# Kernel optimization log

Hardware: AMD Instinct MI355X
Metric: run time of the kernel (lower is better)

Reference implementation:

```python
import jax, jax.numpy as jnp
import numpy as np

L, B, S, H, NH, FF = 4, 16, 512, 768, 12, 3072
D = H // NH
SCALE = D ** -0.5
EPS = 1e-5


def _ln(x, g, b):
    m = jnp.mean(x, axis=-1, keepdims=True)
    v = jnp.mean((x - m) ** 2, axis=-1, keepdims=True)
    return (x - m) * jax.lax.rsqrt(v + EPS) * g + b


def setup_inputs() -> dict:
    key = jax.random.key(0)
    ks = jax.random.split(key, 16)
    def n(k, shape, s=0.02):
        return jax.random.normal(k, shape, dtype=jnp.float32) * s
    return {
        "x": jax.random.normal(ks[0], (B, S, H), dtype=jnp.float32),
        "attn_bias": jax.random.normal(ks[1], (B, NH, S, S), dtype=jnp.float32) * 0.1,
        "ln1_g": jnp.ones((L, H), jnp.float32), "ln1_b": jnp.zeros((L, H), jnp.float32),
        "wq": n(ks[2], (L, H, H)), "bq": jnp.zeros((L, H), jnp.float32),
        "wk": n(ks[3], (L, H, H)), "bk": jnp.zeros((L, H), jnp.float32),
        "wv": n(ks[4], (L, H, H)), "bv": jnp.zeros((L, H), jnp.float32),
        "wo": n(ks[5], (L, H, H)), "bo": jnp.zeros((L, H), jnp.float32),
        "ln2_g": jnp.ones((L, H), jnp.float32), "ln2_b": jnp.zeros((L, H), jnp.float32),
        "w1": n(ks[6], (L, H, FF)), "b1": jnp.zeros((L, FF), jnp.float32),
        "w2": n(ks[7], (L, FF, H)), "b2": jnp.zeros((L, H), jnp.float32),
        "fln_g": jnp.ones((H,), jnp.float32), "fln_b": jnp.zeros((H,), jnp.float32),
    }


def reference(x, attn_bias, ln1_g, ln1_b, wq, bq, wk, bk, wv, bv, wo, bo,
              ln2_g, ln2_b, w1, b1, w2, b2, fln_g, fln_b):
    def body(h, p):
        l1g, l1b, Wq, Bq, Wk, Bk, Wv, Bv, Wo, Bo, l2g, l2b, W1, B1, W2, B2 = p
        y = _ln(h, l1g, l1b)
        # [B,S,H] -> [B,NH,S,D]
        q = (y @ Wq + Bq).reshape(B, S, NH, D).transpose(0, 2, 1, 3)
        k = (y @ Wk + Bk).reshape(B, S, NH, D).transpose(0, 2, 1, 3)
        v = (y @ Wv + Bv).reshape(B, S, NH, D).transpose(0, 2, 1, 3)
        a = jnp.einsum('bhsd,bhtd->bhst', q * SCALE, k) + attn_bias
        a = jax.nn.softmax(a, axis=-1)
        o = jnp.einsum('bhst,bhtd->bhsd', a, v).transpose(0, 2, 1, 3).reshape(B, S, H)
        h = h + o @ Wo + Bo
        y = _ln(h, l2g, l2b)
        y = jax.nn.gelu(y @ W1 + B1, approximate=False) @ W2 + B2
        return h + y, None

    params = (ln1_g, ln1_b, wq, bq, wk, bk, wv, bv, wo, bo, ln2_g, ln2_b, w1, b1, w2, b2)
    x, _ = jax.lax.scan(body, x, params)
    return _ln(x, fln_g, fln_b)
```

## Files before the change

### kernel.cpp

```cpp
#include <hip/hip_runtime.h>
#include <math.h>

constexpr int Lc = 4, Bc = 16, Sc = 512, Hc = 768, NHc = 12, FFc = 3072, Dc = 64;
constexpr int MR = Bc * Sc;
constexpr int QS = 2304;
constexpr float SCALEc = 0.125f;

typedef __attribute__((ext_vector_type(8))) __bf16 bf16x8;
typedef __attribute__((ext_vector_type(4))) __bf16 bf16x4;
typedef __attribute__((ext_vector_type(4))) float  floatx4;

__device__ inline floatx4 mfma16(bf16x8 a, bf16x8 b, floatx4 c) {
    return __builtin_amdgcn_mfma_f32_16x16x32_bf16(a, b, c, 0, 0, 0);
}
__device__ inline float gelu_f(float x) {
    return 0.5f * x * (1.0f + erff(x * 0.70710678118654752f));
}
__device__ inline void ld16(const __bf16* g, __bf16* l) {
    __builtin_amdgcn_global_load_lds(
        (const __attribute__((address_space(1))) void*)g,
        (__attribute__((address_space(3))) void*)l, 16, 0, 0);
}

template<bool FINAL>
__global__ __launch_bounds__(256) void ln_k(
    const float* __restrict__ x, const float* __restrict__ g, const float* __restrict__ bt,
    __bf16* __restrict__ yb, float* __restrict__ yf)
{
    const int row  = blockIdx.x * 4 + (threadIdx.x >> 6);
    const int lane = threadIdx.x & 63;
    const int col  = lane * 12;
    const float* xr = x + (size_t)row * Hc + col;
    float v[12];
    *(float4*)(v + 0) = *(const float4*)(xr + 0);
    *(float4*)(v + 4) = *(const float4*)(xr + 4);
    *(float4*)(v + 8) = *(const float4*)(xr + 8);
    float s = 0.f, s2 = 0.f;
#pragma unroll
    for (int j = 0; j < 12; ++j) { s += v[j]; s2 += v[j] * v[j]; }
#pragma unroll
    for (int o = 32; o > 0; o >>= 1) { s += __shfl_xor(s, o); s2 += __shfl_xor(s2, o); }
    const float mean = s * (1.0f / Hc);
    const float inv  = rsqrtf(s2 * (1.0f / Hc) - mean * mean + 1e-5f);
    float gv[12], bv[12];
    *(float4*)(gv + 0) = *(const float4*)(g + col);
    *(float4*)(gv + 4) = *(const float4*)(g + col + 4);
    *(float4*)(gv + 8) = *(const float4*)(g + col + 8);
    *(float4*)(bv + 0) = *(const float4*)(bt + col);
    *(float4*)(bv + 4) = *(const float4*)(bt + col + 4);
    *(float4*)(bv + 8) = *(const float4*)(bt + col + 8);
    if (FINAL) {
        float o[12];
#pragma unroll
        for (int j = 0; j < 12; ++j) o[j] = (v[j] - mean) * inv * gv[j] + bv[j];
        float* yr = yf + (size_t)row * Hc + col;
        *(float4*)(yr + 0) = *(float4*)(o + 0);
        *(float4*)(yr + 4) = *(float4*)(o + 4);
        *(float4*)(yr + 8) = *(float4*)(o + 8);
    } else {
        __bf16 o[12];
#pragma unroll
        for (int j = 0; j < 12; ++j) o[j] = (__bf16)((v[j] - mean) * inv * gv[j] + bv[j]);
        __bf16* yr = yb + (size_t)row * Hc + col;
        *(bf16x4*)(yr + 0) = *(bf16x4*)(o + 0);
        *(bf16x4*)(yr + 4) = *(bf16x4*)(o + 4);
        *(bf16x4*)(yr + 8) = *(bf16x4*)(o + 8);
    }
}

__global__ __launch_bounds__(256) void prep_k(
    const float* __restrict__ wq, const float* __restrict__ wk,
    const float* __restrict__ wv, const float* __restrict__ wo,
    const float* __restrict__ w1, const float* __restrict__ w2,
    const float* __restrict__ bq, const float* __restrict__ bk, const float* __restrict__ bv,
    __bf16* __restrict__ wqkvt, __bf16* __restrict__ wot,
    __bf16* __restrict__ w1t, __bf16* __restrict__ w2t, float* __restrict__ bqkv)
{
    const int id = blockIdx.x;
    if (id >= 6912) {
        int i = (id - 6912) * 256 + threadIdx.x;
        if (i < QS) bqkv[i] = i < Hc ? bq[i] : (i < 2 * Hc ? bk[i - Hc] : bv[i - 2 * Hc]);
        return;
    }
    const float* in; __bf16* out; int R, C, tile;
    if (id < 2304) {
        int piece = id / 576; tile = id % 576; R = Hc; C = Hc;
        in  = piece == 0 ? wq : piece == 1 ? wk : piece == 2 ? wv : wo;
        out = piece == 3 ? wot : wqkvt + (size_t)piece * Hc * Hc;
    } else if (id < 4608) {
        tile = id - 2304; R = Hc; C = FFc; in = w1; out = w1t;
    } else {
        tile = id - 4608; R = FFc; C = Hc; in = w2; out = w2t;
    }
    const int nx = C / 32;
    const int bx = tile % nx, by = tile / nx;
    __shared__ float t[32][33];
    const int c0 = bx * 32, r0 = by * 32;
    const int tx = threadIdx.x & 31, ty = threadIdx.x >> 5;
#pragma unroll
    for (int i2 = 0; i2 < 4; ++i2)
        t[ty + i2 * 8][tx] = in[(size_t)(r0 + ty + i2 * 8) * C + c0 + tx];
    __syncthreads();
#pragma unroll
    for (int i2 = 0; i2 < 4; ++i2)
        out[(size_t)(c0 + ty + i2 * 8) * R + r0 + tx] = (__bf16)t[tx][ty + i2 * 8];
}

template<int ACT, bool RESID>
__global__ __launch_bounds__(256) void gemm2_k(
    const __bf16* __restrict__ A, const __bf16* __restrict__ Bt,
    const float* __restrict__ bias, const float* __restrict__ resid,
    float* __restrict__ outF, __bf16* __restrict__ outB,
    int M, int N, int K)
{
    __shared__ alignas(16) __bf16 As[128 * 32];
    __shared__ alignas(16) __bf16 Bs[128 * 32];
    const int tid  = threadIdx.x;
    const int wave = tid >> 6, lane = tid & 63, lhi = lane >> 4, llo = lane & 15;
    const int wm = wave >> 1, wn = wave & 1;
    const int row0 = blockIdx.y * 128, col0 = blockIdx.x * 128;
    const int srow = lane >> 2;
    const int scol = (lane & 3) * 8;

    floatx4 acc[4][4];
#pragma unroll
    for (int i = 0; i < 4; ++i)
#pragma unroll
        for (int j = 0; j < 4; ++j) acc[i][j] = {0.f, 0.f, 0.f, 0.f};

    const __bf16* Ab = A  + (size_t)(row0 + wave * 16 + srow) * K + scol;
    const __bf16* Bb = Bt + (size_t)(col0 + wave * 16 + srow) * K + scol;

    for (int kt = 0; kt < K; kt += 32) {
#pragma unroll
        for (int t = 0; t < 2; ++t) {
            ld16(Ab + (size_t)(t * 64) * K + kt, As + (t * 64 + wave * 16) * 32);
            ld16(Bb + (size_t)(t * 64) * K + kt, Bs + (t * 64 + wave * 16) * 32);
        }
        __syncthreads();
        bf16x8 af[4], bfr[4];
#pragma unroll
        for (int i = 0; i < 4; ++i)
            af[i]  = *(const bf16x8*)(As + (wm * 64 + i * 16 + llo) * 32 + lhi * 8);
#pragma unroll
        for (int j = 0; j < 4; ++j)
            bfr[j] = *(const bf16x8*)(Bs + (wn * 64 + j * 16 + llo) * 32 + lhi * 8);
#pragma unroll
        for (int i = 0; i < 4; ++i)
#pragma unroll
            for (int j = 0; j < 4; ++j)
                acc[i][j] = mfma16(af[i], bfr[j], acc[i][j]);
        __syncthreads();
    }
#pragma unroll
    for (int i = 0; i < 4; ++i) {
#pragma unroll
        for (int j = 0; j < 4; ++j) {
            int colc = col0 + wn * 64 + j * 16 + llo;
            float bb = bias[colc];
#pragma unroll
            for (int r = 0; r < 4; ++r) {
                int rowc = row0 + wm * 64 + i * 16 + lhi * 4 + r;
                float vv = acc[i][j][r] + bb;
                if (ACT == 1) vv = gelu_f(vv);
                size_t idx = (size_t)rowc * N + colc;
                if (RESID) outF[idx] = resid[idx] + vv;
                else       outB[idx] = (__bf16)vv;
            }
        }
    }
}

__global__ __launch_bounds__(256) void gemm3_k(
    const __bf16* __restrict__ A, const __bf16* __restrict__ Bt,
    const float* __restrict__ bias, const float* __restrict__ resid,
    float* __restrict__ outF, int M, int N, int K)
{
    __shared__ alignas(16) __bf16 As[2][128 * 32];
    __shared__ alignas(16) __bf16 Bs[2][64 * 32];
    const int tid  = threadIdx.x;
    const int wave = tid >> 6, lane = tid & 63, lhi = lane >> 4, llo = lane & 15;
    const int row0 = blockIdx.y * 128, col0 = blockIdx.x * 64;
    const int srow = lane >> 2;
    const int scol = (lane & 3) * 8;

    floatx4 acc[2][4];
#pragma unroll
    for (int i = 0; i < 2; ++i)
#pragma unroll
        for (int j = 0; j < 4; ++j) acc[i][j] = {0.f, 0.f, 0.f, 0.f};

    const __bf16* Ab = A  + (size_t)(row0 + wave * 32 + srow) * K + scol;
    const __bf16* Bb = Bt + (size_t)(col0 + wave * 16 + srow) * K + scol;

#define G3_STAGE(buf, kt)                                                      \
    do {                                                                       \
        ld16(Ab + (kt),                   &As[buf][(wave * 32 +  0) * 32]);    \
        ld16(Ab + (size_t)16 * K + (kt),  &As[buf][(wave * 32 + 16) * 32]);    \
        ld16(Bb + (kt),                   &Bs[buf][(wave * 16) * 32]);         \
    } while (0)

    G3_STAGE(0, 0);
    __syncthreads();
    const int nt = K >> 5;
    for (int t = 0; t < nt; ++t) {
        const int cur = t & 1;
        if (t + 1 < nt) G3_STAGE(cur ^ 1, (size_t)(t + 1) * 32);
        bf16x8 af[2], bfr[4];
#pragma unroll
        for (int i = 0; i < 2; ++i)
            af[i]  = *(const bf16x8*)(&As[cur][(wave * 32 + i * 16 + llo) * 32 + lhi * 8]);
#pragma unroll
        for (int j = 0; j < 4; ++j)
            bfr[j] = *(const bf16x8*)(&Bs[cur][(j * 16 + llo) * 32 + lhi * 8]);
#pragma unroll
        for (int i = 0; i < 2; ++i)
#pragma unroll
            for (int j = 0; j < 4; ++j)
                acc[i][j] = mfma16(af[i], bfr[j], acc[i][j]);
        __syncthreads();
    }
#undef G3_STAGE

#pragma unroll
    for (int i = 0; i < 2; ++i) {
#pragma unroll
        for (int j = 0; j < 4; ++j) {
            int colc = col0 + j * 16 + llo;
            float bb = bias[colc];
#pragma unroll
            for (int r = 0; r < 4; ++r) {
                int rowc = row0 + wave * 32 + i * 16 + lhi * 4 + r;
                size_t idx = (size_t)rowc * N + colc;
                outF[idx] = resid[idx] + acc[i][j][r] + bb;
            }
        }
    }
}

__global__ __launch_bounds__(256) void attn_k(
    const __bf16* __restrict__ q, const __bf16* __restrict__ k,
    const __bf16* __restrict__ v, const float* __restrict__ bias,
    __bf16* __restrict__ o)
{
    __shared__ alignas(16) __bf16 QPs[64][72];
    __shared__ alignas(16) __bf16 Ks[2][64][72];
    __shared__ alignas(16) __bf16 Vt[2][64][66];

    const int hh = blockIdx.x % NHc, b = blockIdx.x / NHc, qt = blockIdx.y;
    const int tid = threadIdx.x, wave = tid >> 6, lane = tid & 63;
    const int lhi = lane >> 4, llo = lane & 15;
    const size_t base  = (size_t)b * Sc * QS + hh * Dc;
    const size_t obase = (size_t)b * Sc * Hc + hh * Dc;

    const int sr0 = tid >> 3;
    const int sc0 = (tid & 7) * 8;

    {
        bf16x8 q0 = *(const bf16x8*)(q + base + (size_t)(qt * 64 + sr0) * QS + sc0);
        bf16x8 q1 = *(const bf16x8*)(q + base + (size_t)(qt * 64 + sr0 + 32) * QS + sc0);
        *(bf16x8*)(&QPs[sr0][sc0])      = q0;
        *(bf16x8*)(&QPs[sr0 + 32][sc0]) = q1;
        bf16x8 k0 = *(const bf16x8*)(k + base + (size_t)(sr0) * QS + sc0);
        bf16x8 k1 = *(const bf16x8*)(k + base + (size_t)(sr0 + 32) * QS + sc0);
        *(bf16x8*)(&Ks[0][sr0][sc0])      = k0;
        *(bf16x8*)(&Ks[0][sr0 + 32][sc0]) = k1;
        bf16x8 v0 = *(const bf16x8*)(v + base + (size_t)(sr0) * QS + sc0);
        bf16x8 v1 = *(const bf16x8*)(v + base + (size_t)(sr0 + 32) * QS + sc0);
#pragma unroll
        for (int jj = 0; jj < 8; ++jj) {
            Vt[0][sc0 + jj][sr0]      = v0[jj];
            Vt[0][sc0 + jj][sr0 + 32] = v1[jj];
        }
    }
    __syncthreads();

    bf16x8 aq0 = *(const bf16x8*)(&QPs[wave * 16 + llo][0 * 32 + lhi * 8]);
    bf16x8 aq1 = *(const bf16x8*)(&QPs[wave * 16 + llo][1 * 32 + lhi * 8]);

    float m_reg[4], l_reg[4];
#pragma unroll
    for (int r = 0; r < 4; ++r) { m_reg[r] = -1e30f; l_reg[r] = 0.f; }

    floatx4 acco[4];
#pragma unroll
    for (int j = 0; j < 4; ++j) acco[j] = {0.f, 0.f, 0.f, 0.f};

    const float* brow = bias + ((size_t)(b * NHc + hh) * Sc + qt * 64) * Sc;

    float bnx[4][4];
#pragma unroll
    for (int nf = 0; nf < 4; ++nf)
#pragma unroll
        for (int r = 0; r < 4; ++r)
            bnx[nf][r] = brow[(size_t)(wave * 16 + lhi * 4 + r) * Sc + nf * 16 + llo];

    for (int it = 0; it < 8; ++it) {
        const int cur = it & 1;
        bf16x8 k0, k1, v0, v1;
        if (it < 7) {
            const int ktn = (it + 1) * 64;
            k0 = *(const bf16x8*)(k + base + (size_t)(ktn + sr0) * QS + sc0);
            k1 = *(const bf16x8*)(k + base + (size_t)(ktn + sr0 + 32) * QS + sc0);
            v0 = *(const bf16x8*)(v + base + (size_t)(ktn + sr0) * QS + sc0);
            v1 = *(const bf16x8*)(v + base + (size_t)(ktn + sr0 + 32) * QS + sc0);
        }
        floatx4 accs[4];
#pragma unroll
        for (int j = 0; j < 4; ++j) accs[j] = {0.f, 0.f, 0.f, 0.f};
#pragma unroll
        for (int nf = 0; nf < 4; ++nf) {
            bf16x8 bk2 = *(const bf16x8*)(&Ks[cur][nf * 16 + llo][lhi * 8]);
            accs[nf] = mfma16(aq0, bk2, accs[nf]);
        }
#pragma unroll
        for (int nf = 0; nf < 4; ++nf) {
            bf16x8 bk2 = *(const bf16x8*)(&Ks[cur][nf * 16 + llo][32 + lhi * 8]);
            accs[nf] = mfma16(aq1, bk2, accs[nf]);
        }
        float sv[4][4];
#pragma unroll
        for (int nf = 0; nf < 4; ++nf)
#pragma unroll
            for (int r = 0; r < 4; ++r)
                sv[nf][r] = accs[nf][r] * SCALEc + bnx[nf][r];
        if (it < 7) {
            const int ktn = (it + 1) * 64;
#pragma unroll
            for (int nf = 0; nf < 4; ++nf)
#pragma unroll
                for (int r = 0; r < 4; ++r)
                    bnx[nf][r] = brow[(size_t)(wave * 16 + lhi * 4 + r) * Sc + ktn + nf * 16 + llo];
        }
        float al[4];
#pragma unroll
        for (int r = 0; r < 4; ++r) {
            float mx = fmaxf(fmaxf(sv[0][r], sv[1][r]), fmaxf(sv[2][r], sv[3][r]));
            mx = fmaxf(mx, __shfl_xor(mx, 1));
            mx = fmaxf(mx, __shfl_xor(mx, 2));
            mx = fmaxf(mx, __shfl_xor(mx, 4));
            mx = fmaxf(mx, __shfl_xor(mx, 8));
            float mnew = fmaxf(m_reg[r], mx);
            al[r] = __expf(m_reg[r] - mnew);
            m_reg[r] = mnew;
            float sum = 0.f;
#pragma unroll
            for (int nf = 0; nf < 4; ++nf) {
                float p = __expf(sv[nf][r] - mnew);
                sum += p;
                QPs[wave * 16 + lhi * 4 + r][nf * 16 + llo] = (__bf16)p;
            }
            sum += __shfl_xor(sum, 1);
            sum += __shfl_xor(sum, 2);
            sum += __shfl_xor(sum, 4);
            sum += __shfl_xor(sum, 8);
            l_reg[r] = l_reg[r] * al[r] + sum;
        }
#pragma unroll
        for (int nf = 0; nf < 4; ++nf)
#pragma unroll
            for (int r = 0; r < 4; ++r) acco[nf][r] *= al[r];
#pragma unroll
        for (int kk = 0; kk < 2; ++kk) {
            bf16x8 ap = *(const bf16x8*)(&QPs[wave * 16 + llo][kk * 32 + lhi * 8]);
#pragma unroll
            for (int nf = 0; nf < 4; ++nf) {
                bf16x8 bv2 = *(const bf16x8*)(&Vt[cur][nf * 16 + llo][kk * 32 + lhi * 8]);
                acco[nf] = mfma16(ap, bv2, acco[nf]);
            }
        }
        if (it < 7) {
            *(bf16x8*)(&Ks[cur ^ 1][sr0][sc0])      = k0;
            *(bf16x8*)(&Ks[cur ^ 1][sr0 + 32][sc0]) = k1;
#pragma unroll
            for (int jj = 0; jj < 8; ++jj) {
                Vt[cur ^ 1][sc0 + jj][sr0]      = v0[jj];
                Vt[cur ^ 1][sc0 + jj][sr0 + 32] = v1[jj];
            }
        }
        __syncthreads();
    }
#pragma unroll
    for (int nf = 0; nf < 4; ++nf) {
#pragma unroll
        for (int r = 0; r < 4; ++r) {
            int lr = wave * 16 + lhi * 4 + r;
            float oo = acco[nf][r] / l_reg[r];
            o[obase + (size_t)(qt * 64 + lr) * Hc + nf * 16 + llo] = (__bf16)oo;
        }
    }
}

extern "C" void kernel_launch(void* const* d_in, const int* in_sizes, int n_in,
                              void* d_out, int out_size, void* d_ws, size_t ws_size,
                              hipStream_t stream)
{
    const float* x     = (const float*)d_in[0];
    const float* abias = (const float*)d_in[1];
    const float* ln1g  = (const float*)d_in[2];
    const float* ln1b  = (const float*)d_in[3];
    const float* wq    = (const float*)d_in[4];
    const float* bq    = (const float*)d_in[5];
    const float* wk    = (const float*)d_in[6];
    const float* bk    = (const float*)d_in[7];
    const float* wv    = (const float*)d_in[8];
    const float* bv    = (const float*)d_in[9];
    const float* wo    = (const float*)d_in[10];
    const float* bo    = (const float*)d_in[11];
    const float* ln2g  = (const float*)d_in[12];
    const float* ln2b  = (const float*)d_in[13];
    const float* w1    = (const float*)d_in[14];
    const float* b1    = (const float*)d_in[15];
    const float* w2    = (const float*)d_in[16];
    const float* b2    = (const float*)d_in[17];
    const float* flng  = (const float*)d_in[18];
    const float* flnb  = (const float*)d_in[19];

    float* h = (float*)d_out;
    __bf16* y    = (__bf16*)d_ws;
    __bf16* qkv  = y   + (size_t)MR * Hc;
    __bf16* ob   = qkv + (size_t)MR * QS;
    __bf16* fb   = ob  + (size_t)MR * Hc;
    __bf16* w1t  = fb  + (size_t)MR * FFc;
    __bf16* w2t  = w1t + (size_t)FFc * Hc;
    float*  bqkv = (float*)(w2t + (size_t)Hc * FFc);
    __bf16* wqkvt = fb;
    __bf16* wot   = fb + (size_t)QS * Hc;

    hipMemcpyAsync(h, x, (size_t)MR * Hc * sizeof(float), hipMemcpyDeviceToDevice, stream);

    dim3 blk(256);
    dim3 gLN(MR / 4);
    dim3 gQKV(QS / 128, MR / 128);
    dim3 gP64(Hc / 64, MR / 128);
    dim3 gF(FFc / 128, MR / 128);
    dim3 gA(Bc * NHc, Sc / 64);
    dim3 gPrep(6921);

    for (int l = 0; l < Lc; ++l) {
        const float* wq_l = wq + (size_t)l * Hc * Hc;
        const float* wk_l = wk + (size_t)l * Hc * Hc;
        const float* wv_l = wv + (size_t)l * Hc * Hc;
        const float* wo_l = wo + (size_t)l * Hc * Hc;
        const float* w1_l = w1 + (size_t)l * Hc * FFc;
        const float* w2_l = w2 + (size_t)l * FFc * Hc;

        prep_k<<<gPrep, blk, 0, stream>>>(wq_l, wk_l, wv_l, wo_l, w1_l, w2_l,
                                          bq + l * Hc, bk + l * Hc, bv + l * Hc,
                                          wqkvt, wot, w1t, w2t, bqkv);

        ln_k<false><<<gLN, blk, 0, stream>>>(h, ln1g + l * Hc, ln1b + l * Hc, y, nullptr);
        gemm2_k<0, false><<<gQKV, blk, 0, stream>>>(y, wqkvt, bqkv, nullptr, nullptr, qkv, MR, QS, Hc);
        attn_k<<<gA, blk, 0, stream>>>(qkv, qkv + Hc, qkv + 2 * Hc, abias, ob);
        gemm3_k<<<gP64, blk, 0, stream>>>(ob, wot, bo + l * Hc, h, h, MR, Hc, Hc);
        ln_k<false><<<gLN, blk, 0, stream>>>(h, ln2g + l * Hc, ln2b + l * Hc, y, nullptr);
        gemm2_k<1, false><<<gF, blk, 0, stream>>>(y, w1t, b1 + l * FFc, nullptr, nullptr, fb, MR, FFc, Hc);
        gemm3_k<<<gP64, blk, 0, stream>>>(fb, w2t, b2 + l * Hc, h, h, MR, Hc, FFc);
    }
    ln_k<true><<<gLN, blk, 0, stream>>>(h, flng, flnb, nullptr, h);
}
```

Baseline: 1.625 ms.

## Double-buffer gemm2 loads, use partial vmcnt waits, and swizzle block order

gemm2 gets double-buffered LDS staging, so the next K tile's global-to-LDS loads overlap the current tile's MFMAs. Both gemm kernels replace __syncthreads with explicit s_waitcnt vmcnt(N) plus s_barrier, waiting only for the older stage's loads. A block-index swizzle interleaves blocks across groups of eight to improve L2 reuse. The trade-offs are double the LDS in gemm2, which may lower occupancy, and hand-written waitcnt counts that depend on the exact number of outstanding loads.

```diff
diff --git a/kernel.cpp b/kernel.cpp
--- a/kernel.cpp
+++ b/kernel.cpp
@@ -21,6 +21,12 @@
         (const __attribute__((address_space(1))) void*)g,
         (__attribute__((address_space(3))) void*)l, 16, 0, 0);
 }
+
+#define WAITVM4   asm volatile("s_waitcnt vmcnt(4)" ::: "memory")
+#define WAITVM3   asm volatile("s_waitcnt vmcnt(3)" ::: "memory")
+#define WAITVM0   asm volatile("s_waitcnt vmcnt(0)" ::: "memory")
+#define WAITLGKM0 asm volatile("s_waitcnt lgkmcnt(0)" ::: "memory")
+#define SBAR      __builtin_amdgcn_s_barrier()
 
 template<bool FINAL>
 __global__ __launch_bounds__(256) void ln_k(
@@ -113,12 +119,17 @@
     float* __restrict__ outF, __bf16* __restrict__ outB,
     int M, int N, int K)
 {
-    __shared__ alignas(16) __bf16 As[128 * 32];
-    __shared__ alignas(16) __bf16 Bs[128 * 32];
+    __shared__ alignas(16) __bf16 As[2][128 * 32];
+    __shared__ alignas(16) __bf16 Bs[2][128 * 32];
     const int tid  = threadIdx.x;
     const int wave = tid >> 6, lane = tid & 63, lhi = lane >> 4, llo = lane & 15;
     const int wm = wave >> 1, wn = wave & 1;
-    const int row0 = blockIdx.y * 128, col0 = blockIdx.x * 128;
+
+    const int nxb = gridDim.x, nb = nxb * gridDim.y;
+    const int bid = blockIdx.y * nxb + blockIdx.x;
+    const int swz = (bid & 7) * (nb >> 3) + (bid >> 3);
+    const int row0 = (swz / nxb) * 128, col0 = (swz % nxb) * 128;
+
     const int srow = lane >> 2;
     const int scol = (lane & 3) * 8;
 
@@ -131,27 +142,39 @@
     const __bf16* Ab = A  + (size_t)(row0 + wave * 16 + srow) * K + scol;
     const __bf16* Bb = Bt + (size_t)(col0 + wave * 16 + srow) * K + scol;
 
-    for (int kt = 0; kt < K; kt += 32) {
-#pragma unroll
-        for (int t = 0; t < 2; ++t) {
-            ld16(Ab + (size_t)(t * 64) * K + kt, As + (t * 64 + wave * 16) * 32);
-            ld16(Bb + (size_t)(t * 64) * K + kt, Bs + (t * 64 + wave * 16) * 32);
-        }
-        __syncthreads();
+#define G2_STAGE(buf, kt)                                                      \
+    do {                                                                       \
+        ld16(Ab + (kt),                  &As[buf][(wave * 16) * 32]);          \
+        ld16(Ab + (size_t)64 * K + (kt), &As[buf][(64 + wave * 16) * 32]);     \
+        ld16(Bb + (kt),                  &Bs[buf][(wave * 16) * 32]);          \
+        ld16(Bb + (size_t)64 * K + (kt), &Bs[buf][(64 + wave * 16) * 32]);     \
+    } while (0)
+
+    G2_STAGE(0, 0);
+    const int nt = K >> 5;
+    for (int t = 0; t < nt; ++t) {
+        const int cur = t & 1;
+        if (t + 1 < nt) { G2_STAGE(cur ^ 1, (size_t)(t + 1) * 32); WAITVM4; }
+        else            { WAITVM0; }
+        SBAR;
+        __builtin_amdgcn_sched_barrier(0);
         bf16x8 af[4], bfr[4];
 #pragma unroll
         for (int i = 0; i < 4; ++i)
-            af[i]  = *(const bf16x8*)(As + (wm * 64 + i * 16 + llo) * 32 + lhi * 8);
+            af[i]  = *(const bf16x8*)(&As[cur][(wm * 64 + i * 16 + llo) * 32 + lhi * 8]);
 #pragma unroll
         for (int j = 0; j < 4; ++j)
-            bfr[j] = *(const bf16x8*)(Bs + (wn * 64 + j * 16 + llo) * 32 + lhi * 8);
+            bfr[j] = *(const bf16x8*)(&Bs[cur][(wn * 64 + j * 16 + llo) * 32 + lhi * 8]);
 #pragma unroll
         for (int i = 0; i < 4; ++i)
 #pragma unroll
             for (int j = 0; j < 4; ++j)
                 acc[i][j] = mfma16(af[i], bfr[j], acc[i][j]);
-        __syncthreads();
-    }
+        WAITLGKM0;
+        SBAR;
+    }
+#undef G2_STAGE
+
 #pragma unroll
     for (int i = 0; i < 4; ++i) {
 #pragma unroll
@@ -180,7 +203,12 @@
     __shared__ alignas(16) __bf16 Bs[2][64 * 32];
     const int tid  = threadIdx.x;
     const int wave = tid >> 6, lane = tid & 63, lhi = lane >> 4, llo = lane & 15;
-    const int row0 = blockIdx.y * 128, col0 = blockIdx.x * 64;
+
+    const int nxb = gridDim.x, nb = nxb * gridDim.y;
+    const int bid = blockIdx.y * nxb + blockIdx.x;
+    const int swz = (bid & 7) * (nb >> 3) + (bid >> 3);
+    const int row0 = (swz / nxb) * 128, col0 = (swz % nxb) * 64;
+
     const int srow = lane >> 2;
     const int scol = (lane & 3) * 8;
 
@@ -195,17 +223,19 @@
 
 #define G3_STAGE(buf, kt)                                                      \
     do {                                                                       \
-        ld16(Ab + (kt),                   &As[buf][(wave * 32 +  0) * 32]);    \
-        ld16(Ab + (size_t)16 * K + (kt),  &As[buf][(wave * 32 + 16) * 32]);    \
-        ld16(Bb + (kt),                   &Bs[buf][(wave * 16) * 32]);         \
+        ld16(Ab + (kt),                  &As[buf][(wave * 32 +  0) * 32]);     \
+        ld16(Ab + (size_t)16 * K + (kt), &As[buf][(wave * 32 + 16) * 32]);     \
+        ld16(Bb + (kt),                  &Bs[buf][(wave * 16) * 32]);          \
     } while (0)
 
     G3_STAGE(0, 0);
-    __syncthreads();
     const int nt = K >> 5;
     for (int t = 0; t < nt; ++t) {
         const int cur = t & 1;
-        if (t + 1 < nt) G3_STAGE(cur ^ 1, (size_t)(t + 1) * 32);
+        if (t + 1 < nt) { G3_STAGE(cur ^ 1, (size_t)(t + 1) * 32); WAITVM3; }
+        else            { WAITVM0; }
+        SBAR;
+        __builtin_amdgcn_sched_barrier(0);
         bf16x8 af[2], bfr[4];
 #pragma unroll
         for (int i = 0; i < 2; ++i)
@@ -218,7 +248,8 @@
 #pragma unroll
             for (int j = 0; j < 4; ++j)
                 acc[i][j] = mfma16(af[i], bfr[j], acc[i][j]);
-        __syncthreads();
+        WAITLGKM0;
+        SBAR;
     }
 #undef G3_STAGE
 
```

Measured after the change: 1.543 ms. -5.1%, faster.
